# Kernel tuning notes

Hardware: AMD Instinct MI355X
Metric: run time of the kernel (lower is better)

The kernel has to match this reference:

```python
import jax, jax.numpy as jnp
import numpy as np
from jax import lax

LOG2PI = float(np.log(2.0 * np.pi))
T, B, H, W, C = 64, 128, 64, 64, 3
A, LSTM_HID, LIN, CH, AH = 3, 512, 512, 256, 256
LSTM_IN = LIN + A + 1 + 1 + 1  # feats + last_action + last_reward + contact + time_till_end


def setup_inputs():
    key = jax.random.key(0)
    ks = jax.random.split(key, 32)

    def rn(i, shape, scale=1.0):
        return jax.random.normal(ks[i], shape, jnp.float32) * scale

    return {
        "x": rn(0, (T * B, H, W, C)),
        "done": jax.random.randint(ks[1], (T * B,), 0, 2, jnp.int32),
        "last_action": rn(2, (T * B, A)),
        "last_reward": rn(3, (T * B, 1)),
        "contact": jax.random.uniform(ks[4], (T * B, 1), jnp.float32),
        "time_till_end": jax.random.uniform(ks[5], (T * B, 1), jnp.float32),
        "action": rn(6, (T * B, A)),
        "h0": rn(7, (1, B, LSTM_HID)),
        "c0": rn(8, (1, B, LSTM_HID)),
        "conv1_w": rn(9, (8, 8, C, 32), 0.05), "conv1_b": jnp.zeros((32,), jnp.float32),
        "conv2_w": rn(10, (4, 4, 32, 64), 0.05), "conv2_b": jnp.zeros((64,), jnp.float32),
        "conv3_w": rn(11, (3, 3, 64, 64), 0.05), "conv3_b": jnp.zeros((64,), jnp.float32),
        "lin_w": rn(12, (1024, LIN), 0.03), "lin_b": jnp.zeros((LIN,), jnp.float32),
        "w_ih": rn(13, (4 * LSTM_HID, LSTM_IN), 0.02),
        "w_hh": rn(14, (4 * LSTM_HID, LSTM_HID), 0.02),
        "b_ih": jnp.zeros((4 * LSTM_HID,), jnp.float32),
        "b_hh": jnp.zeros((4 * LSTM_HID,), jnp.float32),
        "critic_w1": rn(15, (LSTM_HID, CH), 0.04), "critic_b1": jnp.zeros((CH,), jnp.float32),
        "critic_w2": rn(16, (CH, CH), 0.06), "critic_b2": jnp.zeros((CH,), jnp.float32),
        "critic_w3": rn(17, (CH, 1), 0.06), "critic_b3": jnp.zeros((1,), jnp.float32),
        "actor_w1": rn(18, (LSTM_HID, AH), 0.04), "actor_b1": jnp.zeros((AH,), jnp.float32),
        "actor_w2": rn(19, (AH, AH), 0.06), "actor_b2": jnp.zeros((AH,), jnp.float32),
        "actor_w3": rn(20, (AH, A), 0.01), "actor_b3": jnp.zeros((A,), jnp.float32),
        "actor_logstd": jnp.zeros((1, A), jnp.float32),
    }


def _conv(x, w, b, stride):
    y = lax.conv_general_dilated(x, w, (stride, stride), "VALID",
                                 dimension_numbers=("NHWC", "HWIO", "NHWC"))
    return jax.nn.relu(y + b)


def _mlp(v, w1, b1, w2, b2, w3, b3):
    v = jnp.tanh(v @ w1 + b1)
    v = jnp.tanh(v @ w2 + b2)
    return v @ w3 + b3


def reference(x, done, last_action, last_reward, contact, time_till_end, action, h0, c0,
              conv1_w, conv1_b, conv2_w, conv2_b, conv3_w, conv3_b, lin_w, lin_b,
              w_ih, w_hh, b_ih, b_hh,
              critic_w1, critic_b1, critic_w2, critic_b2, critic_w3, critic_b3,
              actor_w1, actor_b1, actor_w2, actor_b2, actor_w3, actor_b3, actor_logstd):
    batch = h0.shape[1]
    # CNN encoder (DQN-style)
    h = _conv(x, conv1_w, conv1_b, 4)            # [TB,15,15,32]
    h = _conv(h, conv2_w, conv2_b, 2)            # [TB,6,6,64]
    h = _conv(h, conv3_w, conv3_b, 1)            # [TB,4,4,64]
    h = h.reshape(h.shape[0], -1)                # [TB,1024]
    h = jax.nn.relu(h @ lin_w + lin_b)           # [TB,512]
    h = jnp.concatenate([h, last_action, last_reward, contact, time_till_end], axis=1)
    steps = h.shape[0] // batch
    xs = h.reshape(steps, batch, -1)             # [T,B,518]
    d = done.astype(h.dtype).reshape(steps, batch)

    def step(carry, inp):
        hs, cs = carry
        xt, dt = inp
        m = (1.0 - dt)[:, None]                  # reset state where done
        hs, cs = hs * m, cs * m
        z = xt @ w_ih.T + b_ih + hs @ w_hh.T + b_hh
        i, f, g, o = jnp.split(z, 4, axis=1)     # torch LSTM gate order i,f,g,o
        cs = jax.nn.sigmoid(f) * cs + jax.nn.sigmoid(i) * jnp.tanh(g)
        hs = jax.nn.sigmoid(o) * jnp.tanh(cs)
        return (hs, cs), hs

    (hN, cN), hid = lax.scan(step, (h0[0], c0[0]), (xs, d))
    hid = hid.reshape(steps * batch, -1)         # [TB,512]

    mean = _mlp(hid, actor_w1, actor_b1, actor_w2, actor_b2, actor_w3, actor_b3)
    logstd = jnp.broadcast_to(actor_logstd, mean.shape)
    inv_var = jnp.exp(-2.0 * logstd)
    logprob = (-0.5 * (action - mean) ** 2 * inv_var - logstd - 0.5 * LOG2PI).sum(axis=1)
    entropy = (0.5 + 0.5 * LOG2PI + logstd).sum(axis=1)
    value = _mlp(hid, critic_w1, critic_b1, critic_w2, critic_b2, critic_w3, critic_b3)
    return logprob, entropy, value, hN[None], cN[None]
```

## Files before the change

### kernel.cpp

```cpp
#include <hip/hip_runtime.h>
#include <hip/hip_bf16.h>
#include <hip/hip_cooperative_groups.h>
#include <cmath>

namespace cg = cooperative_groups;

using bf16 = __hip_bfloat16;

#define DEV static __device__ __forceinline__

DEV float toF(float x) { return x; }
DEV float toF(bf16 x) { return __bfloat162float(x); }

DEV float loadF(const void* p, long i, int f32) {
    return f32 ? ((const float*)p)[i] : toF(((const bf16*)p)[i]);
}
DEV void storeOut(void* out, long i, float v, int f32) {
    if (f32) ((float*)out)[i] = v;
    else ((bf16*)out)[i] = __float2bfloat16(v);
}

__device__ __constant__ float kLOG2PI = 1.8378770664093453f;
DEV float sigf(float x) { return 1.0f / (1.0f + __expf(-x)); }

typedef __attribute__((ext_vector_type(4))) float fx4;
typedef __attribute__((ext_vector_type(8))) short s16x8;

static constexpr size_t OFF_WIHT  = 0;
static constexpr size_t OFF_WHHT  = 2121728;
static constexpr size_t OFF_BSUM  = 4218880;
static constexpr size_t OFF_LINB  = 4227072;
static constexpr size_t OFF_HB    = 4229120;
static constexpr size_t OFF_HT0   = 4233216;
static constexpr size_t OFF_HT1   = 4495360;
static constexpr size_t OFF_CT    = 4757504;
static constexpr size_t OFF_CW1   = 5019648;
static constexpr size_t OFF_CW2   = 5031936;
static constexpr size_t OFF_CW3   = 5097472;
static constexpr size_t OFF_CBIAS = 5171200;
static constexpr size_t OFF_ACT   = 5171840;
static constexpr size_t OFF_FB    = 5220992;
static constexpr size_t OFF_FLAG  = 5221024;
static constexpr size_t OFF_XIN   = 5221120;
static constexpr size_t OFF_C3H   = 13708032;
static constexpr size_t OFF_HID   = 22096640;
static constexpr size_t OFF_OUT2 = OFF_C3H;
static constexpr size_t OFF_OUT3 = OFF_C3H + 2359296;
static constexpr size_t OFF_LINW = OFF_C3H + 3407872;
static constexpr size_t OFF_OUT1 = OFF_HID;

__global__ void detect_k(const void* __restrict__ action, int* __restrict__ flag) {
    int lane = threadIdx.x;
    const unsigned short* p = (const unsigned short*)action;
    unsigned short v = p[lane];
    int e = (v >> 7) & 0xFF;
    bool bad = (e >= 0x8C);
    unsigned long long m = __ballot(bad);
    if (lane == 0) *flag = (m != 0ull) ? 1 : 0;
}

__global__ __launch_bounds__(256) void prep_k(
    const void* w_ih, const void* w_hh, const void* b_ih, const void* b_hh,
    const void* lin_b, const void* ab1, const void* ab2, const void* cb1, const void* cb2,
    const void* h0, const void* c0,
    const void* c1w, const void* c2w, const void* c3w,
    const void* c1b, const void* c2b, const void* c3b,
    const void* action, const void* ab3, const void* cb3, const void* logstd,
    bf16* __restrict__ wihT, bf16* __restrict__ whhT,
    float* __restrict__ bsum, float* __restrict__ linbf, float* __restrict__ hbias,
    bf16* __restrict__ h0b, float* __restrict__ cT,
    bf16* __restrict__ cw1, bf16* __restrict__ cw2, bf16* __restrict__ cw3,
    float* __restrict__ cbias, bf16* __restrict__ act, float* __restrict__ fb,
    const int* __restrict__ flagp,
    const void* lin_w, bf16* __restrict__ linwb)
{
    const int f = *flagp;
    long i = (long)blockIdx.x * 256 + threadIdx.x;
    if (i < 1060864) { long k = i >> 11, j = i & 2047;
        wihT[i] = __float2bfloat16(loadF(w_ih, j * 518 + k, f)); return; }
    i -= 1060864;
    if (i < 1048576) { long k = i >> 11, j = i & 2047;
        whhT[i] = __float2bfloat16(loadF(w_hh, j * 512 + k, f)); return; }
    i -= 1048576;
    if (i < 2048) { bsum[i] = loadF(b_ih, i, f) + loadF(b_hh, i, f); return; }
    i -= 2048;
    if (i < 512)  { linbf[i] = loadF(lin_b, i, f); return; }
    i -= 512;
    if (i < 1024) { int w = (int)(i >> 8), r = (int)(i & 255);
        const void* s = (w == 0) ? ab1 : (w == 1) ? ab2 : (w == 2) ? cb1 : cb2;
        hbias[i] = loadF(s, r, f); return; }
    i -= 1024;
    if (i < 65536) { h0b[i] = __float2bfloat16(loadF(h0, i, f)); return; }
    i -= 65536;
    if (i < 65536) { long b = i & 127, k = i >> 7; cT[i]  = loadF(c0, b * 512 + k, f); return; }
    i -= 65536;
    if (i < 6144)  { cw1[i] = __float2bfloat16(loadF(c1w, i, f)); return; }
    i -= 6144;
    if (i < 32768) { cw2[i] = __float2bfloat16(loadF(c2w, i, f)); return; }
    i -= 32768;
    if (i < 36864) { cw3[i] = __float2bfloat16(loadF(c3w, i, f)); return; }
    i -= 36864;
    if (i < 160) { float v = (i < 32) ? loadF(c1b, i, f)
                         : (i < 96) ? loadF(c2b, i - 32, f) : loadF(c3b, i - 96, f);
        cbias[i] = v; return; }
    i -= 160;
    if (i < 24576) { act[i] = __float2bfloat16(loadF(action, i, f)); return; }
    i -= 24576;
    if (i < 8) {
        float v = 0.f;
        if (i < 3) v = loadF(ab3, i, f);
        else if (i == 3) v = loadF(cb3, 0, f);
        else if (i < 7) v = loadF(logstd, i - 4, f);
        fb[i] = v; return;
    }
    i -= 8;
    if (i < 524288) { linwb[i] = __float2bfloat16(loadF(lin_w, i, f)); return; }
}

template <int BN, int MODE, int BSRC = 0, int IC = 1, int KX = 1, int ST = 1,
          int IW = 1, int OW = 1, int OHW = 1>
__global__ __launch_bounds__(256) void mfma_gemm(
    const void* __restrict__ A, int lda,
    const void* __restrict__ B, int ldb,
    const float* __restrict__ bias,
    bf16* __restrict__ C, int ldc,
    int M, int N, int K, int ACT,
    const int* __restrict__ flagp, int imgBase)
{
    constexpr int BM = 128;
    constexpr int LSTR = 40;
    __shared__ __align__(16) bf16 As[BM * LSTR];
    __shared__ __align__(16) bf16 Bs[BN * LSTR];

    const int tid = threadIdx.x;
    const int lane = tid & 63, wave = tid >> 6;
    const int row0 = blockIdx.y * BM, col0 = blockIdx.x * BN;

    constexpr int NWN = (BN >= 64) ? 2 : 1;
    constexpr int WM = BM / (4 / NWN);
    constexpr int WN = BN / NWN;
    constexpr int FM = WM / 16, FN = WN / 16;
    const int wm = (wave / NWN) * WM;
    const int wn = (wave % NWN) * WN;

    fx4 acc[FM][FN] = {};

    const int am = tid >> 1;
    const int ak = (tid & 1) * 16;
    const int gm = row0 + am;
    int ibase = 0;
    if constexpr (MODE != 0) {
        int img = imgBase + gm / OHW;
        int s = gm % OHW;
        int oy = s / OW, ox = s % OW;
        ibase = (img * IW + oy * ST) * IW + ox * ST;
    }
    const int f32f = (MODE == 1 || BSRC == 1) ? *flagp : 0;

    constexpr int KPT = BN / 8;
    const int nloc = tid & (BN - 1);
    const int kg0 = (tid / BN) * KPT;

    for (int k0 = 0; k0 < K; k0 += 32) {
        {
            bf16 tb[16];
            const int kk0 = k0 + ak;
            if constexpr (MODE == 0) {
                const unsigned short* Ab = (const unsigned short*)A + (long)gm * lda;
                if (kk0 + 16 <= K) {
                    const unsigned int* s4 = (const unsigned int*)(Ab + kk0);
                    unsigned int* d4 = (unsigned int*)tb;
                    #pragma unroll
                    for (int j = 0; j < 8; ++j) d4[j] = s4[j];
                } else {
                    unsigned short* bs = (unsigned short*)tb;
                    #pragma unroll
                    for (int j = 0; j < 16; ++j) {
                        int kg = kk0 + j;
                        bs[j] = (kg < K) ? Ab[kg] : (unsigned short)0;
                    }
                }
            } else {
                #pragma unroll
                for (int j = 0; j < 16; ++j) {
                    int kg = kk0 + j;
                    int ky = kg / (KX * IC);
                    int rem = kg - ky * (KX * IC);
                    int kx = rem / IC;
                    int ic = rem - kx * IC;
                    long idx = (long)(ibase + ky * IW + kx) * IC + ic;
                    if constexpr (MODE == 1)
                        tb[j] = __float2bfloat16(loadF(A, idx, f32f));
                    else
                        tb[j] = ((const bf16*)A)[idx];
                }
            }
            unsigned int* dst = (unsigned int*)(As + am * LSTR + ak);
            const unsigned int* src = (const unsigned int*)tb;
            #pragma unroll
            for (int j = 0; j < 8; ++j) dst[j] = src[j];
        }
        {
            bf16 tb[KPT];
            #pragma unroll
            for (int j = 0; j < KPT; ++j) {
                int kg = k0 + kg0 + j;
                if constexpr (BSRC == 1) {
                    float v = 0.f;
                    if (kg < K) v = loadF(B, (long)kg * ldb + col0 + nloc, f32f);
                    tb[j] = __float2bfloat16(v);
                } else {
                    unsigned short v = 0;
                    if (kg < K) v = ((const unsigned short*)B)[(long)kg * ldb + col0 + nloc];
                    ((unsigned short*)tb)[j] = v;
                }
            }
            unsigned int* dst = (unsigned int*)(Bs + nloc * LSTR + kg0);
            const unsigned int* src = (const unsigned int*)tb;
            #pragma unroll
            for (int j = 0; j < KPT / 2; ++j) dst[j] = src[j];
        }
        __syncthreads();

        const int lr = lane & 15, lc = (lane >> 4) * 8;
        s16x8 af[FM], bfr[FN];
        #pragma unroll
        for (int i = 0; i < FM; ++i)
            af[i] = *(const s16x8*)(As + (wm + i * 16 + lr) * LSTR + lc);
        #pragma unroll
        for (int j = 0; j < FN; ++j)
            bfr[j] = *(const s16x8*)(Bs + (wn + j * 16 + lr) * LSTR + lc);
        #pragma unroll
        for (int i = 0; i < FM; ++i)
            #pragma unroll
            for (int j = 0; j < FN; ++j)
                acc[i][j] = __builtin_amdgcn_mfma_f32_16x16x32_bf16(
                    af[i], bfr[j], acc[i][j], 0, 0, 0);
        __syncthreads();
    }

    const int er = (lane >> 4) * 4, ec = lane & 15;
    #pragma unroll
    for (int i = 0; i < FM; ++i) {
        #pragma unroll
        for (int j = 0; j < FN; ++j) {
            const int cc = col0 + wn + j * 16 + ec;
            const float bv = bias[cc];
            #pragma unroll
            for (int r = 0; r < 4; ++r) {
                int rr = row0 + wm + i * 16 + er + r;
                float v = acc[i][j][r] + bv;
                if (ACT == 1) v = fmaxf(v, 0.f);
                if (ACT == 2) v = tanhf(v);
                C[(long)rr * ldc + cc] = __float2bfloat16(v);
            }
        }
    }
}

__global__ __launch_bounds__(256) void concat_k(
    const void* __restrict__ la, const void* __restrict__ lr,
    const void* __restrict__ ct, const void* __restrict__ tte,
    bf16* __restrict__ xin, const int* __restrict__ flagp)
{
    const int f = *flagp;
    int i = blockIdx.x * 256 + threadIdx.x;
    if (i >= 8192 * 6) return;
    int n = i / 6, e = i % 6;
    float v;
    if (e < 3) v = loadF(la, (long)n * 3 + e, f);
    else if (e == 3) v = loadF(lr, n, f);
    else if (e == 4) v = loadF(ct, n, f);
    else v = loadF(tte, n, f);
    xin[(size_t)n * 518 + 512 + e] = __float2bfloat16(v);
}

__global__ __launch_bounds__(256, 1) void lstm16_k(
    const bf16* __restrict__ zx,
    const bf16* __restrict__ whhT,
    const int* __restrict__ done,
    const bf16* __restrict__ h0b,
    bf16* __restrict__ hid,
    float* __restrict__ cT,
    int chunk)
{
    __shared__ float zsm[128][17];
    const int tid = threadIdx.x;
    const int lane = tid & 63, wave = tid >> 6;
    const int bk = blockIdx.x;
    const int c0 = bk * 4;

    const int q = lane & 15;
    const int gcol = (q >> 2) * 512 + c0 + (q & 3);
    const int kb = (lane >> 4) * 8;

    s16x8 bfrag[16];
    #pragma unroll
    for (int kt = 0; kt < 16; ++kt) {
        #pragma unroll
        for (int j = 0; j < 8; ++j) {
            int k = kt * 32 + kb + j;
            ((short*)&bfrag[kt])[j] = ((const short*)whhT)[(long)k * 2048 + gcol];
        }
    }

    float creg[2];
    #pragma unroll
    for (int r = 0; r < 2; ++r) {
        int p = tid + r * 256;
        int b = p >> 2, cc = p & 3;
        creg[r] = cT[(c0 + cc) * 128 + b];
    }

    const int m0 = wave * 32;
    const int lr16 = lane & 15;
    cg::grid_group grid = cg::this_grid();

    for (int ts = 0; ts < 16; ++ts) {
        const int gt = chunk * 16 + ts;
        const bf16* hsrc = (gt == 0) ? h0b : (hid + (long)(gt - 1) * 65536);

        fx4 acc0 = {}, acc1 = {};
        #pragma unroll
        for (int kt = 0; kt < 16; ++kt) {
            s16x8 a0 = *(const s16x8*)(hsrc + (long)(m0 + lr16) * 512 + kt * 32 + kb);
            s16x8 a1 = *(const s16x8*)(hsrc + (long)(m0 + 16 + lr16) * 512 + kt * 32 + kb);
            acc0 = __builtin_amdgcn_mfma_f32_16x16x32_bf16(a0, bfrag[kt], acc0, 0, 0, 0);
            acc1 = __builtin_amdgcn_mfma_f32_16x16x32_bf16(a1, bfrag[kt], acc1, 0, 0, 0);
        }
        const int er = (lane >> 4) * 4;
        #pragma unroll
        for (int r = 0; r < 4; ++r) zsm[m0 + er + r][q] = acc0[r];
        #pragma unroll
        for (int r = 0; r < 4; ++r) zsm[m0 + 16 + er + r][q] = acc1[r];
        __syncthreads();

        #pragma unroll
        for (int r = 0; r < 2; ++r) {
            int p = tid + r * 256;
            int b = p >> 2, cc = p & 3;
            float m = done[gt * 128 + b] ? 0.f : 1.f;
            long zrow = (long)((gt & 15) * 128 + b) * 2048 + c0 + cc;
            float zi = toF(zx[zrow])        + m * zsm[b][0 + cc];
            float zf = toF(zx[zrow + 512])  + m * zsm[b][4 + cc];
            float zg = toF(zx[zrow + 1024]) + m * zsm[b][8 + cc];
            float zo = toF(zx[zrow + 1536]) + m * zsm[b][12 + cc];
            float ig = sigf(zi), fg = sigf(zf), og = sigf(zo);
            float gg = tanhf(zg);
            float cn = fg * (creg[r] * m) + ig * gg;
            float hn = og * tanhf(cn);
            creg[r] = cn;
            hid[(long)(gt * 128 + b) * 512 + c0 + cc] = __float2bfloat16(hn);
        }
        __threadfence();
        grid.sync();
    }

    #pragma unroll
    for (int r = 0; r < 2; ++r) {
        int p = tid + r * 256;
        int b = p >> 2, cc = p & 3;
        cT[(c0 + cc) * 128 + b] = creg[r];
    }
}

__global__ __launch_bounds__(256) void actor_final(
    const bf16* __restrict__ t2, const void* __restrict__ w3,
    const bf16* __restrict__ act, const float* __restrict__ fb,
    void* __restrict__ out, const int* __restrict__ flagp)
{
    const int f = *flagp;
    int lane = threadIdx.x & 63;
    int n = blockIdx.x * 4 + (threadIdx.x >> 6);
    const bf16* row = t2 + (size_t)n * 256;
    float s0 = 0.f, s1 = 0.f, s2 = 0.f;
    #pragma unroll
    for (int j = 0; j < 4; ++j) {
        int k = lane + j * 64;
        float v = toF(row[k]);
        s0 += v * loadF(w3, (long)k * 3 + 0, f);
        s1 += v * loadF(w3, (long)k * 3 + 1, f);
        s2 += v * loadF(w3, (long)k * 3 + 2, f);
    }
    #pragma unroll
    for (int off = 32; off > 0; off >>= 1) {
        s0 += __shfl_down(s0, off, 64);
        s1 += __shfl_down(s1, off, 64);
        s2 += __shfl_down(s2, off, 64);
    }
    if (lane == 0) {
        float mean[3] = {s0 + fb[0], s1 + fb[1], s2 + fb[2]};
        float lp = 0.f, ent = 0.f;
        #pragma unroll
        for (int a = 0; a < 3; ++a) {
            float ls = fb[4 + a];
            float iv = __expf(-2.f * ls);
            float d = toF(act[n * 3 + a]) - mean[a];
            lp += -0.5f * d * d * iv - ls - 0.5f * kLOG2PI;
            ent += 0.5f + 0.5f * kLOG2PI + ls;
        }
        storeOut(out, n, lp, f);
        storeOut(out, 8192 + n, ent, f);
    }
}

__global__ __launch_bounds__(256) void critic_final(
    const bf16* __restrict__ t2, const void* __restrict__ w3,
    const float* __restrict__ fb, void* __restrict__ out,
    const int* __restrict__ flagp)
{
    const int f = *flagp;
    int lane = threadIdx.x & 63;
    int n = blockIdx.x * 4 + (threadIdx.x >> 6);
    const bf16* row = t2 + (size_t)n * 256;
    float s = 0.f;
    #pragma unroll
    for (int j = 0; j < 4; ++j) {
        int k = lane + j * 64;
        s += toF(row[k]) * loadF(w3, k, f);
    }
    #pragma unroll
    for (int off = 32; off > 0; off >>= 1) s += __shfl_down(s, off, 64);
    if (lane == 0) storeOut(out, 16384 + n, s + fb[3], f);
}

__global__ __launch_bounds__(256) void state_out_k(
    const bf16* __restrict__ hid, const float* __restrict__ cT,
    void* __restrict__ out, const int* __restrict__ flagp)
{
    const int f = *flagp;
    int i = blockIdx.x * 256 + threadIdx.x;
    if (i >= 65536) return;
    int b = i >> 9, k = i & 511;
    storeOut(out, 24576 + i, toF(hid[4128768 + i]), f);
    storeOut(out, 90112 + i, cT[k * 128 + b], f);
}

extern "C" void kernel_launch(void* const* d_in, const int* in_sizes, int n_in,
                              void* d_out, int out_size, void* d_ws, size_t ws_size,
                              hipStream_t stream)
{
    const void* x        = d_in[0];
    const int*  done     = (const int*)d_in[1];
    const void* last_act = d_in[2];
    const void* last_rew = d_in[3];
    const void* contact  = d_in[4];
    const void* tte      = d_in[5];
    const void* action   = d_in[6];
    const void* h0       = d_in[7];
    const void* c0       = d_in[8];
    const void* conv1_w  = d_in[9],  *conv1_b = d_in[10];
    const void* conv2_w  = d_in[11], *conv2_b = d_in[12];
    const void* conv3_w  = d_in[13], *conv3_b = d_in[14];
    const void* lin_w    = d_in[15], *lin_b   = d_in[16];
    const void* w_ih     = d_in[17], *w_hh    = d_in[18];
    const void* b_ih     = d_in[19], *b_hh    = d_in[20];
    const void* critic_w1 = d_in[21], *critic_b1 = d_in[22];
    const void* critic_w2 = d_in[23], *critic_b2 = d_in[24];
    const void* critic_w3 = d_in[25], *critic_b3 = d_in[26];
    const void* actor_w1  = d_in[27], *actor_b1  = d_in[28];
    const void* actor_w2  = d_in[29], *actor_b2  = d_in[30];
    const void* actor_w3  = d_in[31], *actor_b3  = d_in[32];
    const void* logstd    = d_in[33];

    char* ws = (char*)d_ws;
    bf16*  wihT  = (bf16*)(ws + OFF_WIHT);
    bf16*  whhT  = (bf16*)(ws + OFF_WHHT);
    float* bsum  = (float*)(ws + OFF_BSUM);
    float* linbf = (float*)(ws + OFF_LINB);
    float* hb    = (float*)(ws + OFF_HB);
    float* ab1f = hb + 0, *ab2f = hb + 256, *cb1f = hb + 512, *cb2f = hb + 768;
    bf16*  h0b = (bf16*)(ws + OFF_HT0);
    float* cT  = (float*)(ws + OFF_CT);
    bf16*  cw1 = (bf16*)(ws + OFF_CW1);
    bf16*  cw2 = (bf16*)(ws + OFF_CW2);
    bf16*  cw3 = (bf16*)(ws + OFF_CW3);
    float* cbias = (float*)(ws + OFF_CBIAS);
    bf16*  act = (bf16*)(ws + OFF_ACT);
    float* fb  = (float*)(ws + OFF_FB);
    int*   flagp = (int*)(ws + OFF_FLAG);
    bf16*  xin = (bf16*)(ws + OFF_XIN);
    bf16*  zxb = (bf16*)(ws + OFF_C3H);
    bf16*  hid = (bf16*)(ws + OFF_HID);
    bf16*  t1b = (bf16*)(ws + OFF_XIN);
    bf16*  t2b = (bf16*)(ws + OFF_C3H);
    bf16*  out1  = (bf16*)(ws + OFF_OUT1);
    bf16*  out2  = (bf16*)(ws + OFF_OUT2);
    bf16*  out3  = (bf16*)(ws + OFF_OUT3);
    bf16*  linwb = (bf16*)(ws + OFF_LINW);

    detect_k<<<1, 64, 0, stream>>>(action, flagp);

    prep_k<<<11207, 256, 0, stream>>>(w_ih, w_hh, b_ih, b_hh, lin_b,
        actor_b1, actor_b2, critic_b1, critic_b2, h0, c0,
        conv1_w, conv2_w, conv3_w, conv1_b, conv2_b, conv3_b,
        action, actor_b3, critic_b3, logstd,
        wihT, whhT, bsum, linbf, hb, h0b, cT, cw1, cw2, cw3, cbias, act, fb, flagp,
        lin_w, linwb);

    for (int c = 0; c < 16; ++c) {
        const int ib = c * 512;
        mfma_gemm<32, 1, 0, 3, 8, 4, 64, 15, 225><<<dim3(1, 900), 256, 0, stream>>>(
            x, 0, cw1, 32, cbias, out1, 32, 115200, 32, 192, 1, flagp, ib);
        mfma_gemm<64, 2, 0, 32, 4, 2, 15, 6, 36><<<dim3(1, 144), 256, 0, stream>>>(
            out1, 0, cw2, 64, cbias + 32, out2, 64, 18432, 64, 512, 1, flagp, 0);
        mfma_gemm<64, 2, 0, 64, 3, 1, 6, 4, 16><<<dim3(1, 64), 256, 0, stream>>>(
            out2, 0, cw3, 64, cbias + 96, out3, 64, 8192, 64, 576, 1, flagp, 0);
        mfma_gemm<64, 0><<<dim3(8, 4), 256, 0, stream>>>(
            out3, 1024, linwb, 512, linbf,
            xin + (size_t)ib * 518, 518, 512, 512, 1024, 1, flagp, 0);
    }
    concat_k<<<192, 256, 0, stream>>>(last_act, last_rew, contact, tte, xin, flagp);

    for (int chunk = 0; chunk < 4; ++chunk) {
        mfma_gemm<64, 0><<<dim3(32, 16), 256, 0, stream>>>(
            xin + (size_t)chunk * 2048 * 518, 518, wihT, 2048, bsum,
            zxb, 2048, 2048, 2048, 518, 0, flagp, 0);
        {
            const bf16* zxp = zxb;
            const bf16* whp = whhT;
            const int*  dnp = done;
            const bf16* h0p = h0b;
            bf16* hip = hid;
            float* ctp = cT;
            int ck = chunk;
            void* args[] = { (void*)&zxp, (void*)&whp, (void*)&dnp, (void*)&h0p,
                             (void*)&hip, (void*)&ctp, (void*)&ck };
            hipLaunchCooperativeKernel(reinterpret_cast<void*>(lstm16_k),
                                       dim3(128), dim3(256), args, 0, stream);
        }
    }

    mfma_gemm<64, 0, 1><<<dim3(4, 64), 256, 0, stream>>>(
        hid, 512, actor_w1, 256, ab1f, t1b, 256, 8192, 256, 512, 2, flagp, 0);
    mfma_gemm<64, 0, 1><<<dim3(4, 64), 256, 0, stream>>>(
        t1b, 256, actor_w2, 256, ab2f, t2b, 256, 8192, 256, 256, 2, flagp, 0);
    actor_final<<<2048, 256, 0, stream>>>(t2b, actor_w3, act, fb, d_out, flagp);

    mfma_gemm<64, 0, 1><<<dim3(4, 64), 256, 0, stream>>>(
        hid, 512, critic_w1, 256, cb1f, t1b, 256, 8192, 256, 512, 2, flagp, 0);
    mfma_gemm<64, 0, 1><<<dim3(4, 64), 256, 0, stream>>>(
        t1b, 256, critic_w2, 256, cb2f, t2b, 256, 8192, 256, 256, 2, flagp, 0);
    critic_final<<<2048, 256, 0, stream>>>(t2b, critic_w3, fb, d_out, flagp);

    state_out_k<<<256, 256, 0, stream>>>(hid, cT, d_out, flagp);
}
```

Before: 6.860 ms.

## Shrink LSTM recurrence grid to 32 blocks with W_hh slices in LDS

The cooperative LSTM kernel now runs 32 blocks instead of 128. Each block owns 16 hidden units across all four gates and keeps its W_hh slice in shared memory, with the weight matrix repacked per block in the prep kernel. Gate math is applied straight from the MFMA accumulators, so the LDS staging buffer and the block barrier inside each step go away. The aim is a cheaper grid-wide sync with fewer blocks, paid for with four times more MFMA and LDS work per block on a serial critical path.

```diff
diff --git a/kernel.cpp b/kernel.cpp
--- a/kernel.cpp
+++ b/kernel.cpp
@@ -79,8 +79,10 @@
     if (i < 1060864) { long k = i >> 11, j = i & 2047;
         wihT[i] = __float2bfloat16(loadF(w_ih, j * 518 + k, f)); return; }
     i -= 1060864;
-    if (i < 1048576) { long k = i >> 11, j = i & 2047;
-        whhT[i] = __float2bfloat16(loadF(w_hh, j * 512 + k, f)); return; }
+    if (i < 1048576) {
+        long bk = i >> 15, q = (i >> 9) & 63, k = i & 511;
+        long col = (q >> 4) * 512 + bk * 16 + (q & 15);
+        whhT[i] = __float2bfloat16(loadF(w_hh, col * 512 + k, f)); return; }
     i -= 1048576;
     if (i < 2048) { bsum[i] = loadF(b_ih, i, f) + loadF(b_hh, i, f); return; }
     i -= 2048;
@@ -277,91 +279,89 @@
 
 __global__ __launch_bounds__(256, 1) void lstm16_k(
     const bf16* __restrict__ zx,
-    const bf16* __restrict__ whhT,
+    const bf16* __restrict__ whhB,
     const int* __restrict__ done,
     const bf16* __restrict__ h0b,
     bf16* __restrict__ hid,
     float* __restrict__ cT,
     int chunk)
 {
-    __shared__ float zsm[128][17];
+    constexpr int LP = 520;
+    __shared__ __align__(16) bf16 Bs[64 * LP];
     const int tid = threadIdx.x;
     const int lane = tid & 63, wave = tid >> 6;
     const int bk = blockIdx.x;
-    const int c0 = bk * 4;
-
-    const int q = lane & 15;
-    const int gcol = (q >> 2) * 512 + c0 + (q & 3);
+    const int lr16 = lane & 15;
     const int kb = (lane >> 4) * 8;
-
-    s16x8 bfrag[16];
-    #pragma unroll
-    for (int kt = 0; kt < 16; ++kt) {
-        #pragma unroll
-        for (int j = 0; j < 8; ++j) {
-            int k = kt * 32 + kb + j;
-            ((short*)&bfrag[kt])[j] = ((const short*)whhT)[(long)k * 2048 + gcol];
-        }
-    }
-
-    float creg[2];
-    #pragma unroll
-    for (int r = 0; r < 2; ++r) {
-        int p = tid + r * 256;
-        int b = p >> 2, cc = p & 3;
-        creg[r] = cT[(c0 + cc) * 128 + b];
-    }
-
+    const int er = (lane >> 4) * 4;
+    const int hc = bk * 16 + lr16;
     const int m0 = wave * 32;
-    const int lr16 = lane & 15;
+
+    {
+        const s16x8* src = (const s16x8*)(whhB + (long)bk * 32768);
+        #pragma unroll
+        for (int it = 0; it < 16; ++it) {
+            int idx = it * 256 + tid;
+            int q = idx >> 6, k8 = (idx & 63) * 8;
+            *(s16x8*)(Bs + q * LP + k8) = src[idx];
+        }
+    }
+
+    float creg[2][4];
+    #pragma unroll
+    for (int mt = 0; mt < 2; ++mt)
+        #pragma unroll
+        for (int r = 0; r < 4; ++r)
+            creg[mt][r] = cT[(long)hc * 128 + (m0 + mt * 16 + er + r)];
+
+    __syncthreads();
     cg::grid_group grid = cg::this_grid();
 
     for (int ts = 0; ts < 16; ++ts) {
         const int gt = chunk * 16 + ts;
         const bf16* hsrc = (gt == 0) ? h0b : (hid + (long)(gt - 1) * 65536);
 
-        fx4 acc0 = {}, acc1 = {};
+        fx4 acc[2][4] = {};
         #pragma unroll
         for (int kt = 0; kt < 16; ++kt) {
             s16x8 a0 = *(const s16x8*)(hsrc + (long)(m0 + lr16) * 512 + kt * 32 + kb);
             s16x8 a1 = *(const s16x8*)(hsrc + (long)(m0 + 16 + lr16) * 512 + kt * 32 + kb);
-            acc0 = __builtin_amdgcn_mfma_f32_16x16x32_bf16(a0, bfrag[kt], acc0, 0, 0, 0);
-            acc1 = __builtin_amdgcn_mfma_f32_16x16x32_bf16(a1, bfrag[kt], acc1, 0, 0, 0);
-        }
-        const int er = (lane >> 4) * 4;
-        #pragma unroll
-        for (int r = 0; r < 4; ++r) zsm[m0 + er + r][q] = acc0[r];
-        #pragma unroll
-        for (int r = 0; r < 4; ++r) zsm[m0 + 16 + er + r][q] = acc1[r];
-        __syncthreads();
-
-        #pragma unroll
-        for (int r = 0; r < 2; ++r) {
-            int p = tid + r * 256;
-            int b = p >> 2, cc = p & 3;
-            float m = done[gt * 128 + b] ? 0.f : 1.f;
-            long zrow = (long)((gt & 15) * 128 + b) * 2048 + c0 + cc;
-            float zi = toF(zx[zrow])        + m * zsm[b][0 + cc];
-            float zf = toF(zx[zrow + 512])  + m * zsm[b][4 + cc];
-            float zg = toF(zx[zrow + 1024]) + m * zsm[b][8 + cc];
-            float zo = toF(zx[zrow + 1536]) + m * zsm[b][12 + cc];
-            float ig = sigf(zi), fg = sigf(zf), og = sigf(zo);
-            float gg = tanhf(zg);
-            float cn = fg * (creg[r] * m) + ig * gg;
-            float hn = og * tanhf(cn);
-            creg[r] = cn;
-            hid[(long)(gt * 128 + b) * 512 + c0 + cc] = __float2bfloat16(hn);
+            #pragma unroll
+            for (int g = 0; g < 4; ++g) {
+                s16x8 bf = *(const s16x8*)(Bs + (g * 16 + lr16) * LP + kt * 32 + kb);
+                acc[0][g] = __builtin_amdgcn_mfma_f32_16x16x32_bf16(a0, bf, acc[0][g], 0, 0, 0);
+                acc[1][g] = __builtin_amdgcn_mfma_f32_16x16x32_bf16(a1, bf, acc[1][g], 0, 0, 0);
+            }
+        }
+
+        #pragma unroll
+        for (int mt = 0; mt < 2; ++mt) {
+            #pragma unroll
+            for (int r = 0; r < 4; ++r) {
+                const int b = m0 + mt * 16 + er + r;
+                const float m = done[gt * 128 + b] ? 0.f : 1.f;
+                const long zr = (long)((gt & 15) * 128 + b) * 2048 + hc;
+                float zi = toF(zx[zr])        + m * acc[mt][0][r];
+                float zf = toF(zx[zr + 512])  + m * acc[mt][1][r];
+                float zg = toF(zx[zr + 1024]) + m * acc[mt][2][r];
+                float zo = toF(zx[zr + 1536]) + m * acc[mt][3][r];
+                float ig = sigf(zi), fg = sigf(zf), og = sigf(zo);
+                float gg = tanhf(zg);
+                float cn = fg * (creg[mt][r] * m) + ig * gg;
+                float hn = og * tanhf(cn);
+                creg[mt][r] = cn;
+                hid[(long)(gt * 128 + b) * 512 + hc] = __float2bfloat16(hn);
+            }
         }
         __threadfence();
         grid.sync();
     }
 
     #pragma unroll
-    for (int r = 0; r < 2; ++r) {
-        int p = tid + r * 256;
-        int b = p >> 2, cc = p & 3;
-        cT[(c0 + cc) * 128 + b] = creg[r];
-    }
+    for (int mt = 0; mt < 2; ++mt)
+        #pragma unroll
+        for (int r = 0; r < 4; ++r)
+            cT[(long)hc * 128 + (m0 + mt * 16 + er + r)] = creg[mt][r];
 }
 
 __global__ __launch_bounds__(256) void actor_final(
@@ -527,7 +527,7 @@
             void* args[] = { (void*)&zxp, (void*)&whp, (void*)&dnp, (void*)&h0p,
                              (void*)&hip, (void*)&ctp, (void*)&ck };
             hipLaunchCooperativeKernel(reinterpret_cast<void*>(lstm16_k),
-                                       dim3(128), dim3(256), args, 0, stream);
+                                       dim3(32), dim3(256), args, 0, stream);
         }
     }
 
```

Result: faster. 5.527 ms (-19.4%).

## Replace LSTM grid sync with per-batch-group counters and LDS-resident weight slices

Applied to the files above, without the earlier changes.

The recurrent LSTM kernel is repartitioned so each of the 128 blocks handles a 16-row batch group and a 32-column hidden slice across all four gates, with that W_hh slice pre-permuted by the prep kernel and staged in shared memory. The grid-wide cooperative sync at every timestep is replaced by per-group atomic counters: a block only waits for the 16 blocks producing its batch group's previous hidden state. This is meant to remove full-grid barrier latency on the serial recurrence, at the cost of spin-wait polling, a large LDS footprint and reliance on correct acquire/release ordering across blocks.

```diff
diff --git a/kernel.cpp b/kernel.cpp
--- a/kernel.cpp
+++ b/kernel.cpp
@@ -41,6 +41,7 @@
 static constexpr size_t OFF_ACT   = 5171840;
 static constexpr size_t OFF_FB    = 5220992;
 static constexpr size_t OFF_FLAG  = 5221024;
+static constexpr size_t OFF_CNT   = 5221056;
 static constexpr size_t OFF_XIN   = 5221120;
 static constexpr size_t OFF_C3H   = 13708032;
 static constexpr size_t OFF_HID   = 22096640;
@@ -49,8 +50,10 @@
 static constexpr size_t OFF_LINW = OFF_C3H + 3407872;
 static constexpr size_t OFF_OUT1 = OFF_HID;
 
-__global__ void detect_k(const void* __restrict__ action, int* __restrict__ flag) {
+__global__ void detect_k(const void* __restrict__ action, int* __restrict__ flag,
+                         unsigned* __restrict__ cnt) {
     int lane = threadIdx.x;
+    if (lane < 8) cnt[lane] = 0u;
     const unsigned short* p = (const unsigned short*)action;
     unsigned short v = p[lane];
     int e = (v >> 7) & 0xFF;
@@ -79,8 +82,11 @@
     if (i < 1060864) { long k = i >> 11, j = i & 2047;
         wihT[i] = __float2bfloat16(loadF(w_ih, j * 518 + k, f)); return; }
     i -= 1060864;
-    if (i < 1048576) { long k = i >> 11, j = i & 2047;
-        whhT[i] = __float2bfloat16(loadF(w_hh, j * 512 + k, f)); return; }
+    if (i < 1048576) {
+        long l = i >> 16, rem = i & 65535;
+        long t = rem >> 13, c = (rem >> 9) & 15, k = rem & 511;
+        long col = (t >> 1) * 512 + l * 32 + (t & 1) * 16 + c;
+        whhT[i] = __float2bfloat16(loadF(w_hh, col * 512 + k, f)); return; }
     i -= 1048576;
     if (i < 2048) { bsum[i] = loadF(b_ih, i, f) + loadF(b_hh, i, f); return; }
     i -= 2048;
@@ -277,30 +283,33 @@
 
 __global__ __launch_bounds__(256, 1) void lstm16_k(
     const bf16* __restrict__ zx,
-    const bf16* __restrict__ whhT,
+    const bf16* __restrict__ whhS,
     const int* __restrict__ done,
     const bf16* __restrict__ h0b,
     bf16* __restrict__ hid,
     float* __restrict__ cT,
+    unsigned* __restrict__ cnt,
     int chunk)
 {
-    __shared__ float zsm[128][17];
+    constexpr int LP = 520;
+    __shared__ __align__(16) bf16 Bs[128 * LP];
+    __shared__ float zsm[16][132];
     const int tid = threadIdx.x;
     const int lane = tid & 63, wave = tid >> 6;
     const int bk = blockIdx.x;
-    const int c0 = bk * 4;
-
-    const int q = lane & 15;
-    const int gcol = (q >> 2) * 512 + c0 + (q & 3);
+    const int g = bk >> 4;
+    const int l = bk & 15;
+    const int lr16 = lane & 15;
     const int kb = (lane >> 4) * 8;
-
-    s16x8 bfrag[16];
-    #pragma unroll
-    for (int kt = 0; kt < 16; ++kt) {
-        #pragma unroll
-        for (int j = 0; j < 8; ++j) {
-            int k = kt * 32 + kb + j;
-            ((short*)&bfrag[kt])[j] = ((const short*)whhT)[(long)k * 2048 + gcol];
+    const int er = (lane >> 4) * 4;
+
+    {
+        const s16x8* src = (const s16x8*)(whhS + (long)l * 65536);
+        #pragma unroll
+        for (int it = 0; it < 32; ++it) {
+            int idx = it * 256 + tid;
+            int row = idx >> 6, k8 = (idx & 63) * 8;
+            *(s16x8*)(Bs + row * LP + k8) = src[idx];
         }
     }
 
@@ -308,59 +317,78 @@
     #pragma unroll
     for (int r = 0; r < 2; ++r) {
         int p = tid + r * 256;
-        int b = p >> 2, cc = p & 3;
-        creg[r] = cT[(c0 + cc) * 128 + b];
-    }
-
-    const int m0 = wave * 32;
-    const int lr16 = lane & 15;
-    cg::grid_group grid = cg::this_grid();
+        int b = g * 16 + (p >> 5), hc = l * 32 + (p & 31);
+        creg[r] = cT[(long)hc * 128 + b];
+    }
+    __syncthreads();
+
+    const bf16* arow0 = h0b + (long)(g * 16 + lr16) * 512;
 
     for (int ts = 0; ts < 16; ++ts) {
         const int gt = chunk * 16 + ts;
-        const bf16* hsrc = (gt == 0) ? h0b : (hid + (long)(gt - 1) * 65536);
-
-        fx4 acc0 = {}, acc1 = {};
+        if (ts > 0) {
+            if (tid == 0) {
+                const unsigned tgt = 16u * (unsigned)gt;
+                while (__hip_atomic_load(cnt + g, __ATOMIC_ACQUIRE,
+                                         __HIP_MEMORY_SCOPE_AGENT) < tgt)
+                    __builtin_amdgcn_s_sleep(1);
+            }
+            __syncthreads();
+            __threadfence();
+        }
+        const bf16* arow = (gt == 0) ? arow0
+                         : (hid + (long)(gt - 1) * 65536 + (long)(g * 16 + lr16) * 512);
+
+        fx4 acc[2] = {};
         #pragma unroll
         for (int kt = 0; kt < 16; ++kt) {
-            s16x8 a0 = *(const s16x8*)(hsrc + (long)(m0 + lr16) * 512 + kt * 32 + kb);
-            s16x8 a1 = *(const s16x8*)(hsrc + (long)(m0 + 16 + lr16) * 512 + kt * 32 + kb);
-            acc0 = __builtin_amdgcn_mfma_f32_16x16x32_bf16(a0, bfrag[kt], acc0, 0, 0, 0);
-            acc1 = __builtin_amdgcn_mfma_f32_16x16x32_bf16(a1, bfrag[kt], acc1, 0, 0, 0);
-        }
-        const int er = (lane >> 4) * 4;
-        #pragma unroll
-        for (int r = 0; r < 4; ++r) zsm[m0 + er + r][q] = acc0[r];
-        #pragma unroll
-        for (int r = 0; r < 4; ++r) zsm[m0 + 16 + er + r][q] = acc1[r];
+            s16x8 a = *(const s16x8*)(arow + kt * 32 + kb);
+            #pragma unroll
+            for (int tl = 0; tl < 2; ++tl) {
+                const int t = wave * 2 + tl;
+                s16x8 bv = *(const s16x8*)(Bs + (t * 16 + lr16) * LP + kt * 32 + kb);
+                acc[tl] = __builtin_amdgcn_mfma_f32_16x16x32_bf16(a, bv, acc[tl], 0, 0, 0);
+            }
+        }
+        #pragma unroll
+        for (int tl = 0; tl < 2; ++tl) {
+            const int zc = (wave * 2 + tl) * 16 + lr16;
+            #pragma unroll
+            for (int r = 0; r < 4; ++r) zsm[er + r][zc] = acc[tl][r];
+        }
         __syncthreads();
 
         #pragma unroll
         for (int r = 0; r < 2; ++r) {
-            int p = tid + r * 256;
-            int b = p >> 2, cc = p & 3;
-            float m = done[gt * 128 + b] ? 0.f : 1.f;
-            long zrow = (long)((gt & 15) * 128 + b) * 2048 + c0 + cc;
-            float zi = toF(zx[zrow])        + m * zsm[b][0 + cc];
-            float zf = toF(zx[zrow + 512])  + m * zsm[b][4 + cc];
-            float zg = toF(zx[zrow + 1024]) + m * zsm[b][8 + cc];
-            float zo = toF(zx[zrow + 1536]) + m * zsm[b][12 + cc];
+            const int p = tid + r * 256;
+            const int b16 = p >> 5, hcl = p & 31;
+            const int b = g * 16 + b16;
+            const float m = done[gt * 128 + b] ? 0.f : 1.f;
+            const long zr = (long)((gt & 15) * 128 + b) * 2048 + l * 32 + hcl;
+            float zi = toF(zx[zr])        + m * zsm[b16][hcl];
+            float zf = toF(zx[zr + 512])  + m * zsm[b16][32 + hcl];
+            float zg = toF(zx[zr + 1024]) + m * zsm[b16][64 + hcl];
+            float zo = toF(zx[zr + 1536]) + m * zsm[b16][96 + hcl];
             float ig = sigf(zi), fg = sigf(zf), og = sigf(zo);
             float gg = tanhf(zg);
             float cn = fg * (creg[r] * m) + ig * gg;
             float hn = og * tanhf(cn);
             creg[r] = cn;
-            hid[(long)(gt * 128 + b) * 512 + c0 + cc] = __float2bfloat16(hn);
-        }
-        __threadfence();
-        grid.sync();
+            hid[(long)(gt * 128 + b) * 512 + l * 32 + hcl] = __float2bfloat16(hn);
+        }
+        __syncthreads();
+        if (tid == 0) {
+            __threadfence();
+            __hip_atomic_fetch_add(cnt + g, 1u, __ATOMIC_RELEASE,
+                                   __HIP_MEMORY_SCOPE_AGENT);
+        }
     }
 
     #pragma unroll
     for (int r = 0; r < 2; ++r) {
         int p = tid + r * 256;
-        int b = p >> 2, cc = p & 3;
-        cT[(c0 + cc) * 128 + b] = creg[r];
+        int b = g * 16 + (p >> 5), hc = l * 32 + (p & 31);
+        cT[(long)hc * 128 + b] = creg[r];
     }
 }
 
@@ -479,6 +507,7 @@
     bf16*  act = (bf16*)(ws + OFF_ACT);
     float* fb  = (float*)(ws + OFF_FB);
     int*   flagp = (int*)(ws + OFF_FLAG);
+    unsigned* cntp = (unsigned*)(ws + OFF_CNT);
     bf16*  xin = (bf16*)(ws + OFF_XIN);
     bf16*  zxb = (bf16*)(ws + OFF_C3H);
     bf16*  hid = (bf16*)(ws + OFF_HID);
@@ -489,7 +518,7 @@
     bf16*  out3  = (bf16*)(ws + OFF_OUT3);
     bf16*  linwb = (bf16*)(ws + OFF_LINW);
 
-    detect_k<<<1, 64, 0, stream>>>(action, flagp);
+    detect_k<<<1, 64, 0, stream>>>(action, flagp, cntp);
 
     prep_k<<<11207, 256, 0, stream>>>(w_ih, w_hh, b_ih, b_hh, lin_b,
         actor_b1, actor_b2, critic_b1, critic_b2, h0, c0,
@@ -523,9 +552,10 @@
             const bf16* h0p = h0b;
             bf16* hip = hid;
             float* ctp = cT;
+            unsigned* cp = cntp;
             int ck = chunk;
             void* args[] = { (void*)&zxp, (void*)&whp, (void*)&dnp, (void*)&h0p,
-                             (void*)&hip, (void*)&ctp, (void*)&ck };
+                             (void*)&hip, (void*)&ctp, (void*)&cp, (void*)&ck };
             hipLaunchCooperativeKernel(reinterpret_cast<void*>(lstm16_k),
                                        dim3(128), dim3(256), args, 0, stream);
         }
```

Result: faster. 5.721 ms (-16.6%).
